# Kernel optimization log

Measured on AMD Instinct MI355X. Metric: run time of the kernel, lower is better.

## Reference

```python
import jax, jax.numpy as jnp
import numpy as np

GROUPS = 32
HEADS = 8
EPS = 1e-5

def setup_inputs() -> dict:
    key = jax.random.key(0)
    ks = jax.random.split(key, 5)
    C = 512
    x = jax.random.normal(ks[0], (8, C, 32, 32), dtype=jnp.float32)
    gn_w = jnp.ones((C,), dtype=jnp.float32)
    gn_b = jnp.zeros((C,), dtype=jnp.float32)
    qkv_w = jax.random.normal(ks[1], (3 * C, C), dtype=jnp.float32) * 0.02
    qkv_b = jnp.zeros((3 * C,), dtype=jnp.float32)
    proj_w = jax.random.normal(ks[2], (C, C), dtype=jnp.float32) * 0.02
    proj_b = jnp.zeros((C,), dtype=jnp.float32)
    return {"x": x, "gn_w": gn_w, "gn_b": gn_b, "qkv_w": qkv_w,
            "qkv_b": qkv_b, "proj_w": proj_w, "proj_b": proj_b}

def reference(x, gn_w, gn_b, qkv_w, qkv_b, proj_w, proj_b):
    B, C, H, W = x.shape
    d = C // HEADS
    # GroupNorm(32, C)
    xg = x.reshape(B, GROUPS, C // GROUPS, H, W)
    mean = xg.mean(axis=(2, 3, 4), keepdims=True)
    var = xg.var(axis=(2, 3, 4), keepdims=True)
    h = ((xg - mean) * jax.lax.rsqrt(var + EPS)).reshape(B, C, H, W)
    h = h * gn_w[None, :, None, None] + gn_b[None, :, None, None]
    # 1x1 conv QKV == channel matmul
    qkv = jnp.einsum('bchw,oc->bohw', h, qkv_w) + qkv_b[None, :, None, None]
    qkv = qkv.reshape(B, 3, HEADS, d, H * W)
    q, k, v = qkv[:, 0], qkv[:, 1], qkv[:, 2]  # [B, heads, d, HW]
    scale = d ** (-0.5)
    # weight[b,h,q,k] = sum_d q[b,h,d,q] * k[b,h,d,k] * scale
    attn = jax.nn.softmax(jnp.einsum('bhdq,bhdk->bhqk', q, k) * scale, axis=-1)
    # out[b,h,d,q] = sum_k v[b,h,d,k] * attn[b,h,q,k]
    out = jnp.einsum('bhdk,bhqk->bhdq', v, attn).reshape(B, C, H, W)
    out = jnp.einsum('bchw,oc->bohw', out, proj_w) + proj_b[None, :, None, None]
    return out + x
```

## Files before the change

### kernel.cpp

```cpp
#include <hip/hip_runtime.h>
#include <math.h>

#define B_    8
#define C_    512
#define HW_   1024
#define O3_   1536
#define HEADS_ 8
#define D_    64
#define G_    32
#define CPG_  16
#define EPS_  1e-5f
#define M_TOT 8192

#define QSCALE (0.125f * 1.44269504088896f)

typedef __bf16 bf16x8 __attribute__((ext_vector_type(8)));
typedef __bf16 bf16x4 __attribute__((ext_vector_type(4)));
typedef float  f32x4  __attribute__((ext_vector_type(4)));

__device__ __forceinline__ void async_copy16(void* lds, const void* g) {
  __builtin_amdgcn_global_load_lds(
      (const __attribute__((address_space(1))) unsigned int*)g,
      (__attribute__((address_space(3))) unsigned int*)lds, 16, 0, 0);
}

__global__ __launch_bounds__(256) void k_gn(const float* __restrict__ x,
                                            const float* __restrict__ gw,
                                            const float* __restrict__ gb,
                                            __bf16* __restrict__ h,
                                            const float* __restrict__ qw,
                                            const float* __restrict__ pw,
                                            __bf16* __restrict__ qwb,
                                            __bf16* __restrict__ pwb) {
  __shared__ float red[10];
  __shared__ __bf16 T[16 * 1030];
  if (blockIdx.x >= B_ * G_) {
    int i = (blockIdx.x - B_ * G_) * 256 + threadIdx.x;
    if (i < O3_ * C_) qwb[i] = (__bf16)qw[i];
    if (i < C_ * C_)  pwb[i] = (__bf16)pw[i];
    return;
  }
  int bg = blockIdx.x;
  int b = bg >> 5, g = bg & 31;
  const float* xg = x + ((size_t)(b * C_) + g * CPG_) * HW_;
  int tid = threadIdx.x;

  float s = 0.f, ss = 0.f;
  for (int i = tid; i < CPG_ * HW_; i += 256) {
    float v = xg[i];
    s += v; ss += v * v;
  }
  for (int off = 32; off > 0; off >>= 1) {
    s  += __shfl_down(s, off, 64);
    ss += __shfl_down(ss, off, 64);
  }
  int wv = tid >> 6;
  if ((tid & 63) == 0) { red[wv] = s; red[4 + wv] = ss; }
  __syncthreads();
  if (tid == 0) {
    float S  = red[0] + red[1] + red[2] + red[3];
    float SS = red[4] + red[5] + red[6] + red[7];
    float mean = S / (float)(CPG_ * HW_);
    float var  = SS / (float)(CPG_ * HW_) - mean * mean;
    red[8] = mean;
    red[9] = rsqrtf(var + EPS_);
  }
  __syncthreads();
  float mean = red[8], rstd = red[9];

  for (int i = tid; i < CPG_ * HW_; i += 256) {
    int c = i >> 10, hw = i & 1023;
    float ga = gw[g * CPG_ + c], be = gb[g * CPG_ + c];
    float v = xg[i];
    T[c * 1030 + hw] = (__bf16)((v - mean) * rstd * ga + be);
  }
  __syncthreads();

  __bf16* hb = h + (size_t)b * HW_ * C_ + g * CPG_;
  for (int j = tid; j < CPG_ * HW_; j += 256) {
    int hw = j >> 4, c = j & 15;
    hb[(size_t)hw * C_ + c] = T[c * 1030 + hw];
  }
}

#define BK 64
__device__ __forceinline__ void gemm128_core(const __bf16* __restrict__ aBase,
                                             const __bf16* __restrict__ bBase,
                                             __bf16* As, __bf16* Bs,
                                             f32x4 acc[4][4]) {
  int t = threadIdx.x;
  int lane = t & 63;
  int l16 = lane & 15, quad = lane >> 4;
  int wv = t >> 6;
  int wm = (wv >> 1) * 64, wn = (wv & 1) * 64;

  int rsub = lane >> 3;
  int chunk = (lane & 7) ^ rsub;
  const __bf16* ag = aBase + (size_t)(wv * 32 + rsub) * C_ + chunk * 8;
  const __bf16* bg = bBase + (size_t)(wv * 32 + rsub) * C_ + chunk * 8;
  __bf16* la = As + wv * 2048 + lane * 8;
  __bf16* lb = Bs + wv * 2048 + lane * 8;
  int sw = l16 & 7;

  for (int k0 = 0; k0 < C_; k0 += BK) {
#pragma unroll
    for (int s = 0; s < 4; s++) {
      async_copy16(la + s * 512, ag + (size_t)(s * 8) * C_ + k0);
      async_copy16(lb + s * 512, bg + (size_t)(s * 8) * C_ + k0);
    }
    __syncthreads();
#pragma unroll
    for (int h = 0; h < 2; h++) {
      bf16x8 af[4], bf[4];
#pragma unroll
      for (int i = 0; i < 4; i++) {
        af[i] = *(const bf16x8*)(As + (wm + i * 16 + l16) * BK +
                                 ((h * 4 + quad) ^ sw) * 8);
        bf[i] = *(const bf16x8*)(Bs + (wn + i * 16 + l16) * BK +
                                 ((h * 4 + quad) ^ sw) * 8);
      }
#pragma unroll
      for (int i = 0; i < 4; i++)
#pragma unroll
        for (int j = 0; j < 4; j++)
          acc[i][j] = __builtin_amdgcn_mfma_f32_16x16x32_bf16(af[i], bf[j],
                                                              acc[i][j], 0, 0, 0);
    }
    __syncthreads();
  }
}

__global__ __launch_bounds__(256) void k_qkv(const __bf16* __restrict__ h,
                                             const __bf16* __restrict__ w,
                                             const float* __restrict__ bias,
                                             __bf16* __restrict__ y,
                                             __bf16* __restrict__ vT) {
  __shared__ __align__(16) __bf16 As[128 * BK];
  __shared__ __align__(16) __bf16 Bs[128 * BK];
  int m0 = blockIdx.x * 128, n0 = blockIdx.y * 128;
  f32x4 acc[4][4];
#pragma unroll
  for (int i = 0; i < 4; i++)
#pragma unroll
    for (int j = 0; j < 4; j++) acc[i][j] = f32x4{0.f, 0.f, 0.f, 0.f};
  gemm128_core(h + (size_t)m0 * C_, w + (size_t)n0 * C_, As, Bs, acc);

  int lane = threadIdx.x & 63, wv = threadIdx.x >> 6;
  int l16 = lane & 15, quad = lane >> 4;
  int wm = (wv >> 1) * 64, wn = (wv & 1) * 64;

  if (n0 >= 2 * C_) {
    int bb = m0 >> 10;
    int tokBase = (m0 & 1023) + wm + quad * 4;
#pragma unroll
    for (int j = 0; j < 4; j++) {
      int n = n0 + wn + j * 16 + l16;
      int c = n - 2 * C_;
      float bv = bias[n];
      __bf16* vrow = vT + ((size_t)(bb * C_) + c) * HW_;
#pragma unroll
      for (int i = 0; i < 4; i++) {
        bf16x4 pk;
#pragma unroll
        for (int r = 0; r < 4; r++) pk[r] = (__bf16)(acc[i][j][r] + bv);
        *(bf16x4*)(vrow + tokBase + i * 16) = pk;
      }
    }
  } else {
    float sc = (n0 < C_) ? QSCALE : 1.0f;
#pragma unroll
    for (int j = 0; j < 4; j++) {
      int n = n0 + wn + j * 16 + l16;
      float bv = bias[n];
#pragma unroll
      for (int i = 0; i < 4; i++)
#pragma unroll
        for (int r = 0; r < 4; r++) {
          int m = m0 + wm + i * 16 + quad * 4 + r;
          y[(size_t)m * O3_ + n] = (__bf16)((acc[i][j][r] + bv) * sc);
        }
    }
  }
}

__global__ __launch_bounds__(256) void k_attn(const __bf16* __restrict__ y,
                                              const __bf16* __restrict__ vT,
                                              __bf16* __restrict__ ao) {
  __shared__ __align__(16) __bf16 Ks[2][128 * 64];
  __shared__ __align__(16) __bf16 Vt[2][64 * 128];
  __shared__ __align__(16) __bf16 Pp[4][32 * 36];
  int hd = blockIdx.x, b = blockIdx.y, qt = blockIdx.z;
  int t = threadIdx.x;
  int wv = t >> 6, lane = t & 63, l16 = lane & 15, quad = lane >> 4;
  int q0 = qt * 128 + wv * 32;

  const __bf16* base = y + (size_t)(b * HW_) * O3_ + hd * D_;
  const __bf16* kg = base + C_;
  const __bf16* vtg = vT + ((size_t)(b * C_) + hd * D_) * HW_;

  bf16x8 qb[2][2];
#pragma unroll
  for (int qg = 0; qg < 2; qg++)
#pragma unroll
    for (int dh = 0; dh < 2; dh++)
      qb[qg][dh] = *(const bf16x8*)(base + (size_t)(q0 + qg * 16 + l16) * O3_ +
                                    dh * 32 + quad * 8);

  int kRowSub = lane >> 3;
  int kChunk = (lane & 7) ^ (kRowSub & 7);

  auto stage = [&](int kt, int bi) {
#pragma unroll
    for (int s = 0; s < 4; s++) {
      int row = wv * 32 + s * 8 + kRowSub;
      async_copy16(&Ks[bi][(wv * 32 + s * 8) * 64 + lane * 8],
                   kg + (size_t)(kt + row) * O3_ + kChunk * 8);
    }
#pragma unroll
    for (int s = 0; s < 4; s++) {
      int row = wv * 16 + s * 4 + (lane >> 4);
      int c2 = (lane & 15) ^ (row & 15);
      async_copy16(&Vt[bi][(wv * 16 + s * 4) * 128 + lane * 8],
                   vtg + (size_t)row * HW_ + kt + c2 * 8);
    }
  };

  float l_run[2] = {0.f, 0.f};
  f32x4 o_acc[4][2];
#pragma unroll
  for (int dt = 0; dt < 4; dt++)
#pragma unroll
    for (int qg = 0; qg < 2; qg++) o_acc[dt][qg] = f32x4{0.f, 0.f, 0.f, 0.f};

  stage(0, 0);

  for (int step = 0; step < 8; step++) {
    int bi = step & 1;
    asm volatile("s_waitcnt vmcnt(0)\n\ts_barrier" ::: "memory");
    if (step < 7) stage((step + 1) * 128, bi ^ 1);

    const __bf16* ks = Ks[bi];
    const __bf16* vs = Vt[bi];
#pragma unroll
    for (int kh = 0; kh < 4; kh++) {
      f32x4 st[2][2];
#pragma unroll
      for (int tti = 0; tti < 2; tti++) {
        int row = (kh * 2 + tti) * 16 + l16;
        bf16x8 ka0 = *(const bf16x8*)(&ks[row * 64 + ((quad) ^ (l16 & 7)) * 8]);
        bf16x8 ka1 = *(const bf16x8*)(&ks[row * 64 + ((4 + quad) ^ (l16 & 7)) * 8]);
        f32x4 z = {0.f, 0.f, 0.f, 0.f};
        st[tti][0] = __builtin_amdgcn_mfma_f32_16x16x32_bf16(ka0, qb[0][0], z, 0, 0, 0);
        st[tti][0] = __builtin_amdgcn_mfma_f32_16x16x32_bf16(ka1, qb[0][1], st[tti][0], 0, 0, 0);
        st[tti][1] = __builtin_amdgcn_mfma_f32_16x16x32_bf16(ka0, qb[1][0], z, 0, 0, 0);
        st[tti][1] = __builtin_amdgcn_mfma_f32_16x16x32_bf16(ka1, qb[1][1], st[tti][1], 0, 0, 0);
      }
#pragma unroll
      for (int qg = 0; qg < 2; qg++) {
        float rs = 0.f;
#pragma unroll
        for (int tti = 0; tti < 2; tti++)
#pragma unroll
          for (int r = 0; r < 4; r++) {
            float e = __builtin_amdgcn_exp2f(st[tti][qg][r]);
            st[tti][qg][r] = e;
            rs += e;
          }
        l_run[qg] += rs;
      }
#pragma unroll
      for (int qg = 0; qg < 2; qg++)
#pragma unroll
        for (int tti = 0; tti < 2; tti++) {
          bf16x4 pk;
#pragma unroll
          for (int r = 0; r < 4; r++) pk[r] = (__bf16)st[tti][qg][r];
          *(bf16x4*)(&Pp[wv][(qg * 16 + l16) * 36 + tti * 16 + quad * 4]) = pk;
        }
      asm volatile("s_waitcnt lgkmcnt(0)" ::: "memory");
      bf16x8 pb0 = *(const bf16x8*)(&Pp[wv][l16 * 36 + quad * 8]);
      bf16x8 pb1 = *(const bf16x8*)(&Pp[wv][(16 + l16) * 36 + quad * 8]);
#pragma unroll
      for (int dt = 0; dt < 4; dt++) {
        int vpos = ((kh * 4 + quad) ^ l16) * 8;
        bf16x8 va = *(const bf16x8*)(&vs[(dt * 16 + l16) * 128 + vpos]);
        o_acc[dt][0] = __builtin_amdgcn_mfma_f32_16x16x32_bf16(va, pb0, o_acc[dt][0], 0, 0, 0);
        o_acc[dt][1] = __builtin_amdgcn_mfma_f32_16x16x32_bf16(va, pb1, o_acc[dt][1], 0, 0, 0);
      }
    }
    asm volatile("s_barrier" ::: "memory");
  }

#pragma unroll
  for (int qg = 0; qg < 2; qg++) {
    l_run[qg] += __shfl_xor(l_run[qg], 16, 64);
    l_run[qg] += __shfl_xor(l_run[qg], 32, 64);
  }
  float inv0 = 1.f / l_run[0], inv1 = 1.f / l_run[1];

#pragma unroll
  for (int dt = 0; dt < 4; dt++) {
    bf16x4 p0, p1;
#pragma unroll
    for (int r = 0; r < 4; r++) {
      p0[r] = (__bf16)(o_acc[dt][0][r] * inv0);
      p1[r] = (__bf16)(o_acc[dt][1][r] * inv1);
    }
    int ch = hd * D_ + dt * 16 + quad * 4;
    *(bf16x4*)(ao + (size_t)(b * HW_ + q0 + l16) * C_ + ch) = p0;
    *(bf16x4*)(ao + (size_t)(b * HW_ + q0 + 16 + l16) * C_ + ch) = p1;
  }
}

__global__ __launch_bounds__(256) void k_proj(const __bf16* __restrict__ ao,
                                              const __bf16* __restrict__ w,
                                              const float* __restrict__ bias,
                                              const float* __restrict__ x,
                                              float* __restrict__ out) {
  __shared__ __align__(16) __bf16 As[128 * BK];
  __shared__ __align__(16) __bf16 Bs[128 * BK];
  int n0 = blockIdx.x * 128, m0 = blockIdx.y * 128;
  f32x4 acc[4][4];
#pragma unroll
  for (int i = 0; i < 4; i++)
#pragma unroll
    for (int j = 0; j < 4; j++) acc[i][j] = f32x4{0.f, 0.f, 0.f, 0.f};
  gemm128_core(w + (size_t)m0 * C_, ao + (size_t)n0 * C_, As, Bs, acc);

  int lane = threadIdx.x & 63, wv = threadIdx.x >> 6;
  int l16 = lane & 15, quad = lane >> 4;
  int wm = (wv >> 1) * 64, wn = (wv & 1) * 64;
#pragma unroll
  for (int i = 0; i < 4; i++)
#pragma unroll
    for (int r = 0; r < 4; r++) {
      int o = m0 + wm + i * 16 + quad * 4 + r;
      float bv = bias[o];
#pragma unroll
      for (int j = 0; j < 4; j++) {
        int n = n0 + wn + j * 16 + l16;
        int b = n >> 10, hw = n & 1023;
        size_t idx = ((size_t)(b * C_ + o)) * HW_ + hw;
        out[idx] = acc[i][j][r] + bv + x[idx];
      }
    }
}

extern "C" void kernel_launch(void* const* d_in, const int* in_sizes, int n_in,
                              void* d_out, int out_size, void* d_ws, size_t ws_size,
                              hipStream_t stream) {
  const float* x      = (const float*)d_in[0];
  const float* gn_w   = (const float*)d_in[1];
  const float* gn_b   = (const float*)d_in[2];
  const float* qkv_w  = (const float*)d_in[3];
  const float* qkv_b  = (const float*)d_in[4];
  const float* proj_w = (const float*)d_in[5];
  const float* proj_b = (const float*)d_in[6];
  float* out = (float*)d_out;

  char* ws = (char*)d_ws;
  __bf16* h   = (__bf16*)(ws);
  __bf16* qwb = (__bf16*)(ws + 8388608);
  __bf16* pwb = (__bf16*)(ws + 8388608 + 1572864);
  __bf16* yq  = (__bf16*)(ws + 8388608 + 1572864 + 524288);
  __bf16* ao  = (__bf16*)(ws + 8388608 + 1572864 + 524288 + 25165824);
  __bf16* vT  = (__bf16*)(ws + 8388608 + 1572864 + 524288 + 25165824 + 8388608);

  int cvtBlocks = (O3_ * C_ + 255) / 256;
  k_gn  <<<B_ * G_ + cvtBlocks, 256, 0, stream>>>(x, gn_w, gn_b, h,
                                                  qkv_w, proj_w, qwb, pwb);
  k_qkv <<<dim3(M_TOT / 128, O3_ / 128, 1), 256, 0, stream>>>(h, qwb, qkv_b, yq, vT);
  k_attn<<<dim3(HEADS_, B_, 8), 256, 0, stream>>>(yq, vT, ao);
  k_proj<<<dim3(M_TOT / 128, C_ / 128, 1), 256, 0, stream>>>(ao, pwb, proj_b, x, out);
  (void)in_sizes; (void)n_in; (void)out_size; (void)ws_size;
}
```

Before: 166.7 us.

## Vectorize GroupNorm and weight casts, shrink proj tile, drop attention barrier

The GroupNorm kernel now reads x as float4, writes packed bf16x4 into a re-padded LDS tile, and stores the transposed output as bf16x8. The weight-cast blocks convert four floats per thread, so fewer blocks are launched. The projection GEMM switches to an inlined 128x64 tile, doubling the grid to improve CU occupancy on the small output GEMM. A trailing s_barrier in the attention K/V loop is removed to cut sync cost; this risks an LDS race if that barrier was protecting buffer reuse.

```diff
diff --git a/kernel.cpp b/kernel.cpp
--- a/kernel.cpp
+++ b/kernel.cpp
@@ -33,22 +33,32 @@
                                             __bf16* __restrict__ qwb,
                                             __bf16* __restrict__ pwb) {
   __shared__ float red[10];
-  __shared__ __bf16 T[16 * 1030];
+  __shared__ __bf16 T[16 * 1032];
   if (blockIdx.x >= B_ * G_) {
     int i = (blockIdx.x - B_ * G_) * 256 + threadIdx.x;
-    if (i < O3_ * C_) qwb[i] = (__bf16)qw[i];
-    if (i < C_ * C_)  pwb[i] = (__bf16)pw[i];
+    if (i < O3_ * C_ / 4) {
+      float4 v = ((const float4*)qw)[i];
+      bf16x4 o = {(__bf16)v.x, (__bf16)v.y, (__bf16)v.z, (__bf16)v.w};
+      ((bf16x4*)qwb)[i] = o;
+    }
+    if (i < C_ * C_ / 4) {
+      float4 v = ((const float4*)pw)[i];
+      bf16x4 o = {(__bf16)v.x, (__bf16)v.y, (__bf16)v.z, (__bf16)v.w};
+      ((bf16x4*)pwb)[i] = o;
+    }
     return;
   }
   int bg = blockIdx.x;
   int b = bg >> 5, g = bg & 31;
   const float* xg = x + ((size_t)(b * C_) + g * CPG_) * HW_;
+  const float4* xg4 = (const float4*)xg;
   int tid = threadIdx.x;
 
   float s = 0.f, ss = 0.f;
-  for (int i = tid; i < CPG_ * HW_; i += 256) {
-    float v = xg[i];
-    s += v; ss += v * v;
+  for (int i = tid; i < CPG_ * HW_ / 4; i += 256) {
+    float4 v = xg4[i];
+    s += v.x + v.y + v.z + v.w;
+    ss += v.x * v.x + v.y * v.y + v.z * v.z + v.w * v.w;
   }
   for (int off = 32; off > 0; off >>= 1) {
     s  += __shfl_down(s, off, 64);
@@ -68,18 +78,27 @@
   __syncthreads();
   float mean = red[8], rstd = red[9];
 
-  for (int i = tid; i < CPG_ * HW_; i += 256) {
-    int c = i >> 10, hw = i & 1023;
+  for (int i = tid; i < CPG_ * HW_ / 4; i += 256) {
+    int c = i >> 8;
+    int hw4 = (i & 255) * 4;
     float ga = gw[g * CPG_ + c], be = gb[g * CPG_ + c];
-    float v = xg[i];
-    T[c * 1030 + hw] = (__bf16)((v - mean) * rstd * ga + be);
+    float4 v = xg4[i];
+    bf16x4 pk;
+    pk[0] = (__bf16)((v.x - mean) * rstd * ga + be);
+    pk[1] = (__bf16)((v.y - mean) * rstd * ga + be);
+    pk[2] = (__bf16)((v.z - mean) * rstd * ga + be);
+    pk[3] = (__bf16)((v.w - mean) * rstd * ga + be);
+    *(bf16x4*)(&T[c * 1032 + hw4]) = pk;
   }
   __syncthreads();
 
   __bf16* hb = h + (size_t)b * HW_ * C_ + g * CPG_;
-  for (int j = tid; j < CPG_ * HW_; j += 256) {
-    int hw = j >> 4, c = j & 15;
-    hb[(size_t)hw * C_ + c] = T[c * 1030 + hw];
+  for (int j = tid; j < 2 * HW_; j += 256) {
+    int hw = j >> 1, c8 = (j & 1) * 8;
+    bf16x8 v;
+#pragma unroll
+    for (int jj = 0; jj < 8; jj++) v[jj] = T[(c8 + jj) * 1032 + hw];
+    *(bf16x8*)(hb + (size_t)hw * C_ + c8) = v;
   }
 }
 
@@ -288,7 +307,6 @@
         o_acc[dt][1] = __builtin_amdgcn_mfma_f32_16x16x32_bf16(va, pb1, o_acc[dt][1], 0, 0, 0);
       }
     }
-    asm volatile("s_barrier" ::: "memory");
   }
 
 #pragma unroll
@@ -318,18 +336,57 @@
                                               const float* __restrict__ x,
                                               float* __restrict__ out) {
   __shared__ __align__(16) __bf16 As[128 * BK];
-  __shared__ __align__(16) __bf16 Bs[128 * BK];
-  int n0 = blockIdx.x * 128, m0 = blockIdx.y * 128;
-  f32x4 acc[4][4];
+  __shared__ __align__(16) __bf16 Bs[64 * BK];
+  int n0 = blockIdx.x * 64, m0 = blockIdx.y * 128;
+  int t = threadIdx.x;
+  int lane = t & 63, l16 = lane & 15, quad = lane >> 4;
+  int wv = t >> 6;
+  int wm = (wv >> 1) * 64, wn = (wv & 1) * 32;
+
+  int rsub = lane >> 3;
+  int chunk = (lane & 7) ^ rsub;
+  const __bf16* ag = w + (size_t)(m0 + wv * 32 + rsub) * C_ + chunk * 8;
+  const __bf16* bg = ao + (size_t)(n0 + wv * 16 + rsub) * C_ + chunk * 8;
+  __bf16* la = As + wv * 2048 + lane * 8;
+  __bf16* lb = Bs + wv * 1024 + lane * 8;
+  int sw = l16 & 7;
+
+  f32x4 acc[4][2];
 #pragma unroll
   for (int i = 0; i < 4; i++)
 #pragma unroll
-    for (int j = 0; j < 4; j++) acc[i][j] = f32x4{0.f, 0.f, 0.f, 0.f};
-  gemm128_core(w + (size_t)m0 * C_, ao + (size_t)n0 * C_, As, Bs, acc);
-
-  int lane = threadIdx.x & 63, wv = threadIdx.x >> 6;
-  int l16 = lane & 15, quad = lane >> 4;
-  int wm = (wv >> 1) * 64, wn = (wv & 1) * 64;
+    for (int j = 0; j < 2; j++) acc[i][j] = f32x4{0.f, 0.f, 0.f, 0.f};
+
+  for (int k0 = 0; k0 < C_; k0 += BK) {
+#pragma unroll
+    for (int s = 0; s < 4; s++)
+      async_copy16(la + s * 512, ag + (size_t)(s * 8) * C_ + k0);
+#pragma unroll
+    for (int s = 0; s < 2; s++)
+      async_copy16(lb + s * 512, bg + (size_t)(s * 8) * C_ + k0);
+    __syncthreads();
+#pragma unroll
+    for (int h = 0; h < 2; h++) {
+      bf16x8 af[4], bf[2];
+#pragma unroll
+      for (int i = 0; i < 4; i++)
+        af[i] = *(const bf16x8*)(As + (wm + i * 16 + l16) * BK +
+                                 ((h * 4 + quad) ^ sw) * 8);
+#pragma unroll
+      for (int j = 0; j < 2; j++)
+        bf[j] = *(const bf16x8*)(Bs + (wn + j * 16 + l16) * BK +
+                                 ((h * 4 + quad) ^ sw) * 8);
+#pragma unroll
+      for (int i = 0; i < 4; i++)
+#pragma unroll
+        for (int j = 0; j < 2; j++)
+          acc[i][j] = __builtin_amdgcn_mfma_f32_16x16x32_bf16(af[i], bf[j],
+                                                              acc[i][j], 0, 0, 0);
+    }
+    __syncthreads();
+  }
+
+  int bb = n0 >> 10;
 #pragma unroll
   for (int i = 0; i < 4; i++)
 #pragma unroll
@@ -337,10 +394,10 @@
       int o = m0 + wm + i * 16 + quad * 4 + r;
       float bv = bias[o];
 #pragma unroll
-      for (int j = 0; j < 4; j++) {
+      for (int j = 0; j < 2; j++) {
         int n = n0 + wn + j * 16 + l16;
-        int b = n >> 10, hw = n & 1023;
-        size_t idx = ((size_t)(b * C_ + o)) * HW_ + hw;
+        int hw = n & 1023;
+        size_t idx = ((size_t)(bb * C_ + o)) * HW_ + hw;
         out[idx] = acc[i][j][r] + bv + x[idx];
       }
     }
@@ -366,11 +423,11 @@
   __bf16* ao  = (__bf16*)(ws + 8388608 + 1572864 + 524288 + 25165824);
   __bf16* vT  = (__bf16*)(ws + 8388608 + 1572864 + 524288 + 25165824 + 8388608);
 
-  int cvtBlocks = (O3_ * C_ + 255) / 256;
+  int cvtBlocks = (O3_ * C_ / 4 + 255) / 256;
   k_gn  <<<B_ * G_ + cvtBlocks, 256, 0, stream>>>(x, gn_w, gn_b, h,
                                                   qkv_w, proj_w, qwb, pwb);
   k_qkv <<<dim3(M_TOT / 128, O3_ / 128, 1), 256, 0, stream>>>(h, qwb, qkv_b, yq, vT);
   k_attn<<<dim3(HEADS_, B_, 8), 256, 0, stream>>>(yq, vT, ao);
-  k_proj<<<dim3(M_TOT / 128, C_ / 128, 1), 256, 0, stream>>>(ao, pwb, proj_b, x, out);
+  k_proj<<<dim3(M_TOT / 64, C_ / 128, 1), 256, 0, stream>>>(ao, pwb, proj_b, x, out);
   (void)in_sizes; (void)n_in; (void)out_size; (void)ws_size;
 }
```

After: 154.9 us. 1.08x faster.
